# Optimization experiments

Measured on AMD Instinct MI355X. Metric: run time of the kernel, lower is better.

## Reference

```python
import jax, jax.numpy as jnp
import numpy as np

HUMAN_CONF = 0.7
KP_CONF = 0.5
NMS_THR = 0.5


def _cxcywh_to_xyxy(b):
    cx, cy, w, h = b[..., 0], b[..., 1], b[..., 2], b[..., 3]
    return jnp.stack([cx - 0.5 * w, cy - 0.5 * h, cx + 0.5 * w, cy + 0.5 * h], axis=-1)


def _iou_matrix(boxes):  # [Q,4] xyxy -> [Q,Q]
    area = jnp.maximum(boxes[:, 2] - boxes[:, 0], 0) * jnp.maximum(boxes[:, 3] - boxes[:, 1], 0)
    lt = jnp.maximum(boxes[:, None, :2], boxes[None, :, :2])
    rb = jnp.minimum(boxes[:, None, 2:], boxes[None, :, 2:])
    wh = jnp.maximum(rb - lt, 0)
    inter = wh[..., 0] * wh[..., 1]
    union = area[:, None] + area[None, :] - inter
    return inter / jnp.maximum(union, 1e-9)


def _nms(boxes, scores, valid, thr):
    # Greedy NMS over score-sorted boxes; invalid boxes never kept.
    Q = scores.shape[0]
    order = jnp.argsort(jnp.where(valid, scores, -jnp.inf))[::-1]
    b, v = boxes[order], valid[order]
    iou = _iou_matrix(b)
    idxs = jnp.arange(Q)

    def body(sup, i):
        keep_i = v[i] & jnp.logical_not(sup[i])
        sup = sup | (keep_i & (iou[i] > thr) & (idxs != i))
        return sup, keep_i

    _, keeps = jax.lax.scan(body, jnp.zeros(Q, bool), idxs)
    return jnp.zeros(Q, bool).at[order].set(keeps)


def _roi_kps(hm, box, sx, sy):
    # hm: [K,H,W] float, box: [4] int32 (xyxy in image coords).
    # Masked full-map argmax == ROI-crop argmax of the original (outside = -inf).
    K, H, W = hm.shape
    x1 = jnp.maximum((box[0].astype(jnp.float32) * sx).astype(jnp.int32), 0)
    y1 = jnp.maximum((box[1].astype(jnp.float32) * sy).astype(jnp.int32), 0)
    x2 = jnp.minimum((box[2].astype(jnp.float32) * sx).astype(jnp.int32) + 1, W)
    y2 = jnp.minimum((box[3].astype(jnp.float32) * sy).astype(jnp.int32) + 1, H)
    xs, ys = jnp.arange(W), jnp.arange(H)
    mask = ((ys >= y1) & (ys < y2))[:, None] & ((xs >= x1) & (xs < x2))[None, :]
    flat = jnp.where(mask[None], hm, -jnp.inf).reshape(K, -1)
    max_vals = flat.max(-1)
    idx = flat.argmax(-1)
    col = (idx % W).astype(jnp.float32)
    row = (idx // W).astype(jnp.float32)
    kps = jnp.stack([col / sx, row / sy, max_vals], -1)  # [K,3]
    ok = (x2 > x1) & (y2 > y1)
    return jnp.where(ok, kps, 0.0)


def setup_inputs() -> dict:
    key = jax.random.key(0)
    k1, k2, k3 = jax.random.split(key, 3)
    B, Q, K, Hh, Wh = 4, 100, 17, 128, 128
    return {
        "human_logits": jax.random.normal(k1, (B, Q, 2), jnp.float32) * 2.0,
        "pred_boxes": jax.random.uniform(k2, (B, Q, 4), jnp.float32),
        "pred_heatmaps": jax.random.normal(k3, (B, K, Hh, Wh), jnp.float32),
        "img_h": 512,
        "img_w": 512,
    }


def reference(human_logits, pred_boxes, pred_heatmaps, img_h, img_w):
    K, Hh, Wh = pred_heatmaps.shape[1:]
    prob = jax.nn.softmax(human_logits, -1)
    scores = prob.max(-1)          # [B,Q]
    labels = prob.argmax(-1)       # [B,Q]
    scale = jnp.array([img_w, img_h, img_w, img_h], jnp.float32)
    boxes = _cxcywh_to_xyxy(pred_boxes) * scale  # [B,Q,4] image coords
    valid = (labels == 0) & (scores >= HUMAN_CONF)
    keep = jax.vmap(lambda b, s, v: _nms(b, s, v, NMS_THR))(boxes, scores, valid)  # [B,Q] bool
    boxes_int = boxes.astype(jnp.int32)
    sx, sy = Wh / img_w, Hh / img_h
    kps = jax.vmap(lambda hm, bx: jax.vmap(lambda b: _roi_kps(hm, b, sx, sy))(bx))(
        pred_heatmaps, boxes_int)  # [B,Q,K,3]
    conf = kps[..., 2]
    kps = kps.at[..., 2].set(jnp.where(conf < KP_CONF, 0.0, conf))
    keep_f = keep.astype(jnp.float32)
    scores_out = scores * keep_f
    kps_out = kps * keep_f[:, :, None, None]
    boxes_out = boxes_int * keep[:, :, None]
    return scores_out, boxes_out, kps_out, keep
```

## Files before the change

### kernel.cpp

```cpp
#include <hip/hip_runtime.h>
#include <cmath>
#include <cfloat>

constexpr int NB = 4;
constexpr int NQ = 100;
constexpr int NK = 17;
constexpr int NH = 128;
constexpr int NW = 128;

constexpr float HUMAN_CONF = 0.7f;
constexpr float KP_CONF    = 0.5f;
constexpr float NMS_THR    = 0.5f;

constexpr int OFF_BOXES = NB * NQ;
constexpr int OFF_KPS   = NB * NQ * 5;
constexpr int OFF_KEEP  = NB * NQ * 5 + NB * NQ * NK * 3;

__global__ __launch_bounds__(128) void score_nms_kernel(
    const float* __restrict__ logits,
    const float* __restrict__ pboxes,
    const int* __restrict__ img_h_p,
    const int* __restrict__ img_w_p,
    float* __restrict__ out,
    int* __restrict__ wcount,
    int2* __restrict__ wlist)
{
    const int b = blockIdx.x;
    const int t = threadIdx.x;

    __shared__ float sbx[NQ][4];
    __shared__ float ssc[NQ];
    __shared__ unsigned char sval[NQ];
    __shared__ int   sorder[NQ];
    __shared__ float sortb[NQ][4];
    __shared__ float sarea[NQ];
    __shared__ unsigned char ssv[NQ];
    __shared__ unsigned long long smask0[NQ], smask1[NQ];
    __shared__ unsigned long long skmask[2];
    __shared__ unsigned long long svb[2];
    __shared__ unsigned long long swl0;

    {
        float4* kz4 = (float4*)(out + OFF_KPS + b * (NQ * NK * 3));
        const float4 z4 = make_float4(0.0f, 0.0f, 0.0f, 0.0f);
        for (int i = t; i < (NQ * NK * 3) / 4; i += 128) kz4[i] = z4;
    }

    const float iw = (float)img_w_p[0];
    const float ih = (float)img_h_p[0];
    const float sx = (float)NW / iw;
    const float sy = (float)NH / ih;

    if (t < NQ) {
        const float l0 = logits[(b * NQ + t) * 2 + 0];
        const float l1 = logits[(b * NQ + t) * 2 + 1];
        const float m  = fmaxf(l0, l1);
        const float e0 = expf(l0 - m);
        const float e1 = expf(l1 - m);
        const float score = fmaxf(e0, e1) / (e0 + e1);
        const bool  lab0  = (l0 >= l1);

        const float cx = pboxes[(b * NQ + t) * 4 + 0];
        const float cy = pboxes[(b * NQ + t) * 4 + 1];
        const float w  = pboxes[(b * NQ + t) * 4 + 2];
        const float h  = pboxes[(b * NQ + t) * 4 + 3];
        sbx[t][0] = (cx - 0.5f * w) * iw;
        sbx[t][1] = (cy - 0.5f * h) * ih;
        sbx[t][2] = (cx + 0.5f * w) * iw;
        sbx[t][3] = (cy + 0.5f * h) * ih;
        ssc[t]  = score;
        sval[t] = (lab0 && score >= HUMAN_CONF) ? 1 : 0;
    }
    __syncthreads();

    if (t < NQ) {
        const float key = sval[t] ? ssc[t] : -INFINITY;
        int rank = 0;
        for (int j = 0; j < NQ; ++j) {
            const float kj = sval[j] ? ssc[j] : -INFINITY;
            if (kj > key || (kj == key && j > t)) rank++;
        }
        sorder[rank] = t;
    }
    __syncthreads();

    if (t < NQ) {
        const int oi = sorder[t];
        const float x1 = sbx[oi][0], y1 = sbx[oi][1], x2 = sbx[oi][2], y2 = sbx[oi][3];
        sortb[t][0] = x1; sortb[t][1] = y1; sortb[t][2] = x2; sortb[t][3] = y2;
        sarea[t] = fmaxf(x2 - x1, 0.0f) * fmaxf(y2 - y1, 0.0f);
        ssv[t]   = sval[oi];
    }
    __syncthreads();

    if (t < NQ) {
        unsigned long long m0 = 0ull, m1 = 0ull;
        const float ax1 = sortb[t][0], ay1 = sortb[t][1], ax2 = sortb[t][2], ay2 = sortb[t][3];
        const float aa = sarea[t];
        for (int j = 0; j < NQ; ++j) {
            const float lx = fmaxf(ax1, sortb[j][0]);
            const float ly = fmaxf(ay1, sortb[j][1]);
            const float rx = fminf(ax2, sortb[j][2]);
            const float ry = fminf(ay2, sortb[j][3]);
            const float wv = fmaxf(rx - lx, 0.0f);
            const float hv = fmaxf(ry - ly, 0.0f);
            const float inter = wv * hv;
            const float uni = aa + sarea[j] - inter;
            const float iou = inter / fmaxf(uni, 1e-9f);
            if (iou > NMS_THR) {
                if (j < 64) m0 |= 1ull << j; else m1 |= 1ull << (j - 64);
            }
        }
        smask0[t] = m0; smask1[t] = m1;
    }

    {
        const bool sv = (t < NQ) ? (ssv[t] != 0) : false;
        const unsigned long long vb = __ballot(sv);
        if ((t & 63) == 0) svb[t >> 6] = vb;
    }
    __syncthreads();

    if (t == 0) {
        unsigned long long rem0 = svb[0], rem1 = svb[1];
        unsigned long long k0 = 0ull, k1 = 0ull;
        while (rem0 | rem1) {
            int i;
            unsigned long long bit0 = 0ull, bit1 = 0ull;
            if (rem0) { i = __builtin_ctzll(rem0); bit0 = 1ull << i; }
            else      { const int j = __builtin_ctzll(rem1); i = 64 + j; bit1 = 1ull << j; }
            k0 |= bit0; k1 |= bit1;
            rem0 &= ~(smask0[i] | bit0);
            rem1 &= ~(smask1[i] | bit1);
        }
        skmask[0] = k0; skmask[1] = k1;
    }
    __syncthreads();

    int  kp = 0, gi = 0;
    int  x1i = 0, y1i = 0, x2i = 0, y2i = 0;
    bool live = false;

    if (t < NQ) {
        const int oi = sorder[t];
        kp = (t < 64) ? (int)((skmask[0] >> t) & 1ull)
                      : (int)((skmask[1] >> (t - 64)) & 1ull);
        gi = b * NQ + oi;

        out[gi] = ssc[oi] * (float)kp;

        const int bi0 = (int)sbx[oi][0];
        const int bi1 = (int)sbx[oi][1];
        const int bi2 = (int)sbx[oi][2];
        const int bi3 = (int)sbx[oi][3];
        out[OFF_BOXES + gi * 4 + 0] = (float)(bi0 * kp);
        out[OFF_BOXES + gi * 4 + 1] = (float)(bi1 * kp);
        out[OFF_BOXES + gi * 4 + 2] = (float)(bi2 * kp);
        out[OFF_BOXES + gi * 4 + 3] = (float)(bi3 * kp);

        out[OFF_KEEP + gi] = (float)kp;

        x1i = max((int)((float)bi0 * sx), 0);
        y1i = max((int)((float)bi1 * sy), 0);
        x2i = min((int)((float)bi2 * sx) + 1, NW);
        y2i = min((int)((float)bi3 * sy) + 1, NH);
        live = kp && (x2i > x1i) && (y2i > y1i);
    }

    const unsigned long long lm = __ballot(live);
    if (t == 0) swl0 = lm;
    __syncthreads();
    if (t == 64) wcount[b] = __popcll(swl0) + __popcll(lm);
    const int lane = t & 63;
    const unsigned long long below = lm & ((lane ? (1ull << lane) : 1ull) - 1ull);
    const int rank = (t < 64) ? __popcll(below) : __popcll(swl0) + __popcll(below);
    if (live) {
        const int pack = x1i | (y1i << 8) | (x2i << 16) | (y2i << 24);
        wlist[b * NQ + rank] = make_int2(pack, gi);
    }
}

__global__ __launch_bounds__(64) void kps_kernel(
    const float* __restrict__ hm,
    const int* __restrict__ wcount,
    const int2* __restrict__ wlist,
    const int* __restrict__ img_h_p,
    const int* __restrict__ img_w_p,
    float* __restrict__ out)
{
    const int c0 = wcount[0] * NK;
    const int c1 = wcount[1] * NK;
    const int c2 = wcount[2] * NK;
    const int c3 = wcount[3] * NK;
    const int t0 = c0, t1 = c0 + c1, t2 = t1 + c2, T = t2 + c3;

    const int lane = threadIdx.x;
    const float sx = (float)NW / (float)img_w_p[0];
    const float sy = (float)NH / (float)img_h_p[0];

    for (int item = blockIdx.x; item < T; item += gridDim.x) {
        int b, base;
        if (item < t1) { if (item < t0) { b = 0; base = 0;  } else { b = 1; base = t0; } }
        else           { if (item < t2) { b = 2; base = t1; } else { b = 3; base = t2; } }
        const int local = item - base;
        const int r = local / NK;
        const int k = local - r * NK;

        const int2 wl = wlist[b * NQ + r];
        const int x1 = wl.x & 255;
        const int y1 = (wl.x >> 8) & 255;
        const int x2 = (wl.x >> 16) & 255;
        const int y2 = (wl.x >> 24) & 255;
        const int gi = wl.y;

        const float4* __restrict__ b4 =
            (const float4*)(hm + (size_t)(b * NK + k) * (NH * NW));

        const int xa     = x1 & ~3;
        const int C4     = (x2 - xa + 3) >> 2;
        const int R      = y2 - y1;
        const int total4 = R * C4;
        const unsigned M = (C4 > 1) ? (0xFFFFFFFFu / (unsigned)C4 + 1u) : 0u;

        float best = -INFINITY;
        int   bidx = 0x7fffffff;

        auto proc = [&](int idx, float4 v) {
            const int row = (C4 == 1) ? idx : (int)__umulhi((unsigned)idx, M);
            const int xb  = xa + (idx - row * C4) * 4;
            const int g   = (y1 + row) * NW + xb;
            const float v0 = (xb + 0 >= x1 && xb + 0 < x2) ? v.x : -INFINITY;
            const float v1 = (xb + 1 >= x1 && xb + 1 < x2) ? v.y : -INFINITY;
            const float v2 = (xb + 2 >= x1 && xb + 2 < x2) ? v.z : -INFINITY;
            const float v3 = (xb + 3 < x2) ? v.w : -INFINITY;
            if (v0 > best) { best = v0; bidx = g + 0; }
            if (v1 > best) { best = v1; bidx = g + 1; }
            if (v2 > best) { best = v2; bidx = g + 2; }
            if (v3 > best) { best = v3; bidx = g + 3; }
        };
        auto caddr = [&](int idx) {
            const int row = (C4 == 1) ? idx : (int)__umulhi((unsigned)idx, M);
            return (y1 + row) * (NW / 4) + (xa >> 2) + (idx - row * C4);
        };

        int idx = lane;
        for (; idx + 192 < total4; idx += 256) {
            const int a0 = caddr(idx), a1 = caddr(idx + 64), a2 = caddr(idx + 128), a3 = caddr(idx + 192);
            const float4 v0 = b4[a0];
            const float4 v1 = b4[a1];
            const float4 v2 = b4[a2];
            const float4 v3 = b4[a3];
            proc(idx, v0);
            proc(idx + 64, v1);
            proc(idx + 128, v2);
            proc(idx + 192, v3);
        }
        for (; idx < total4; idx += 64) proc(idx, b4[caddr(idx)]);

        for (int off = 32; off >= 1; off >>= 1) {
            const float ov = __shfl_down(best, off);
            const int   oi = __shfl_down(bidx, off);
            if (ov > best || (ov == best && oi < bidx)) { best = ov; bidx = oi; }
        }

        if (lane == 0) {
            const int col = bidx & (NW - 1);
            const int row = bidx >> 7;
            float conf = best;
            if (conf < KP_CONF) conf = 0.0f;
            float* kout = out + OFF_KPS + (size_t)gi * (NK * 3) + k * 3;
            kout[0] = (float)col / sx;
            kout[1] = (float)row / sy;
            kout[2] = conf;
        }
    }
}

extern "C" void kernel_launch(void* const* d_in, const int* in_sizes, int n_in,
                              void* d_out, int out_size, void* d_ws, size_t ws_size,
                              hipStream_t stream) {
    const float* logits = (const float*)d_in[0];
    const float* pboxes = (const float*)d_in[1];
    const float* hm     = (const float*)d_in[2];
    const int*   img_h  = (const int*)d_in[3];
    const int*   img_w  = (const int*)d_in[4];
    float* out = (float*)d_out;

    int*  wcount = (int*)d_ws;
    int2* wlist  = (int2*)((char*)d_ws + 256);

    score_nms_kernel<<<NB, 128, 0, stream>>>(logits, pboxes, img_h, img_w, out, wcount, wlist);
    kps_kernel<<<2048, 64, 0, stream>>>(hm, wcount, wlist, img_h, img_w, out);
}
```

Measured before the change: 106.6 us.

## Fuse scoring/NMS and keypoint ROI argmax into one kernel with redundant per-block NMS

Merges the two kernels into one launch of 1024 blocks. Each block redundantly recomputes softmax, sorting and NMS for its batch, then processes a strided slice of (query, keypoint) items straight from a shared-memory ROI pack table, which removes the workspace handoff and the second launch. Each thread also issues one float4 heatmap load per 64-byte line early to warm the cache while NMS runs. Suppressed queries write zeros directly instead of using a separate zero-fill pass. The cost is NMS duplicated 256 times per batch and a fixed work split that ignores how many boxes are actually live.

```diff
diff --git a/kernel.cpp b/kernel.cpp
--- a/kernel.cpp
+++ b/kernel.cpp
@@ -16,17 +16,21 @@
 constexpr int OFF_KPS   = NB * NQ * 5;
 constexpr int OFF_KEEP  = NB * NQ * 5 + NB * NQ * NK * 3;
 
-__global__ __launch_bounds__(128) void score_nms_kernel(
+constexpr int NBLK = 1024;
+constexpr int WAVES_PER_BATCH = (NBLK / NB) * 2;
+
+__global__ __launch_bounds__(128) void fused_kernel(
     const float* __restrict__ logits,
     const float* __restrict__ pboxes,
+    const float* __restrict__ hm,
     const int* __restrict__ img_h_p,
     const int* __restrict__ img_w_p,
-    float* __restrict__ out,
-    int* __restrict__ wcount,
-    int2* __restrict__ wlist)
+    float* __restrict__ out)
 {
-    const int b = blockIdx.x;
-    const int t = threadIdx.x;
+    const int blk = blockIdx.x;
+    const int t   = threadIdx.x;
+    const int b   = blk & 3;
+    const int sub = blk >> 2;
 
     __shared__ float sbx[NQ][4];
     __shared__ float ssc[NQ];
@@ -38,18 +42,17 @@
     __shared__ unsigned long long smask0[NQ], smask1[NQ];
     __shared__ unsigned long long skmask[2];
     __shared__ unsigned long long svb[2];
-    __shared__ unsigned long long swl0;
-
-    {
-        float4* kz4 = (float4*)(out + OFF_KPS + b * (NQ * NK * 3));
-        const float4 z4 = make_float4(0.0f, 0.0f, 0.0f, 0.0f);
-        for (int i = t; i < (NQ * NK * 3) / 4; i += 128) kz4[i] = z4;
-    }
+    __shared__ int sqpack[NQ];
+
+    float4 wv4 = make_float4(0.f, 0.f, 0.f, 0.f);
+    const int  line = blk * 128 + t;
+    const bool doW  = line < (NB * NK * NH * NW) / 16;
+    if (doW) wv4 = ((const float4*)hm)[line * 4];
 
     const float iw = (float)img_w_p[0];
     const float ih = (float)img_h_p[0];
-    const float sx = (float)NW / iw;
-    const float sy = (float)NH / ih;
+    const float sxl = (float)NW / iw;
+    const float syl = (float)NH / ih;
 
     if (t < NQ) {
         const float l0 = logits[(b * NQ + t) * 2 + 0];
@@ -137,81 +140,57 @@
     }
     __syncthreads();
 
-    int  kp = 0, gi = 0;
-    int  x1i = 0, y1i = 0, x2i = 0, y2i = 0;
-    bool live = false;
-
     if (t < NQ) {
         const int oi = sorder[t];
-        kp = (t < 64) ? (int)((skmask[0] >> t) & 1ull)
-                      : (int)((skmask[1] >> (t - 64)) & 1ull);
-        gi = b * NQ + oi;
-
-        out[gi] = ssc[oi] * (float)kp;
+        const int kp = (t < 64) ? (int)((skmask[0] >> t) & 1ull)
+                                : (int)((skmask[1] >> (t - 64)) & 1ull);
 
         const int bi0 = (int)sbx[oi][0];
         const int bi1 = (int)sbx[oi][1];
         const int bi2 = (int)sbx[oi][2];
         const int bi3 = (int)sbx[oi][3];
-        out[OFF_BOXES + gi * 4 + 0] = (float)(bi0 * kp);
-        out[OFF_BOXES + gi * 4 + 1] = (float)(bi1 * kp);
-        out[OFF_BOXES + gi * 4 + 2] = (float)(bi2 * kp);
-        out[OFF_BOXES + gi * 4 + 3] = (float)(bi3 * kp);
-
-        out[OFF_KEEP + gi] = (float)kp;
-
-        x1i = max((int)((float)bi0 * sx), 0);
-        y1i = max((int)((float)bi1 * sy), 0);
-        x2i = min((int)((float)bi2 * sx) + 1, NW);
-        y2i = min((int)((float)bi3 * sy) + 1, NH);
-        live = kp && (x2i > x1i) && (y2i > y1i);
-    }
-
-    const unsigned long long lm = __ballot(live);
-    if (t == 0) swl0 = lm;
-    __syncthreads();
-    if (t == 64) wcount[b] = __popcll(swl0) + __popcll(lm);
+
+        const int x1i = max((int)((float)bi0 * sxl), 0);
+        const int y1i = max((int)((float)bi1 * syl), 0);
+        const int x2i = min((int)((float)bi2 * sxl) + 1, NW);
+        const int y2i = min((int)((float)bi3 * syl) + 1, NH);
+        const bool live = kp && (x2i > x1i) && (y2i > y1i);
+
+        sqpack[oi] = live ? (x1i | (y1i << 8) | (x2i << 16) | (y2i << 24)) : 0;
+
+        if (sub == 0) {
+            const int gi = b * NQ + oi;
+            out[gi] = ssc[oi] * (float)kp;
+            out[OFF_BOXES + gi * 4 + 0] = (float)(bi0 * kp);
+            out[OFF_BOXES + gi * 4 + 1] = (float)(bi1 * kp);
+            out[OFF_BOXES + gi * 4 + 2] = (float)(bi2 * kp);
+            out[OFF_BOXES + gi * 4 + 3] = (float)(bi3 * kp);
+            out[OFF_KEEP + gi] = (float)kp;
+        }
+    }
+    __syncthreads();
+
+    if (doW) asm volatile("" :: "v"(wv4.x), "v"(wv4.y), "v"(wv4.z), "v"(wv4.w));
+
     const int lane = t & 63;
-    const unsigned long long below = lm & ((lane ? (1ull << lane) : 1ull) - 1ull);
-    const int rank = (t < 64) ? __popcll(below) : __popcll(swl0) + __popcll(below);
-    if (live) {
-        const int pack = x1i | (y1i << 8) | (x2i << 16) | (y2i << 24);
-        wlist[b * NQ + rank] = make_int2(pack, gi);
-    }
-}
-
-__global__ __launch_bounds__(64) void kps_kernel(
-    const float* __restrict__ hm,
-    const int* __restrict__ wcount,
-    const int2* __restrict__ wlist,
-    const int* __restrict__ img_h_p,
-    const int* __restrict__ img_w_p,
-    float* __restrict__ out)
-{
-    const int c0 = wcount[0] * NK;
-    const int c1 = wcount[1] * NK;
-    const int c2 = wcount[2] * NK;
-    const int c3 = wcount[3] * NK;
-    const int t0 = c0, t1 = c0 + c1, t2 = t1 + c2, T = t2 + c3;
-
-    const int lane = threadIdx.x;
-    const float sx = (float)NW / (float)img_w_p[0];
-    const float sy = (float)NH / (float)img_h_p[0];
-
-    for (int item = blockIdx.x; item < T; item += gridDim.x) {
-        int b, base;
-        if (item < t1) { if (item < t0) { b = 0; base = 0;  } else { b = 1; base = t0; } }
-        else           { if (item < t2) { b = 2; base = t1; } else { b = 3; base = t2; } }
-        const int local = item - base;
-        const int r = local / NK;
-        const int k = local - r * NK;
-
-        const int2 wl = wlist[b * NQ + r];
-        const int x1 = wl.x & 255;
-        const int y1 = (wl.x >> 8) & 255;
-        const int x2 = (wl.x >> 16) & 255;
-        const int y2 = (wl.x >> 24) & 255;
-        const int gi = wl.y;
+    const int wvid = sub * 2 + (t >> 6);
+
+    for (int item = wvid; item < NQ * NK; item += WAVES_PER_BATCH) {
+        const int q = item / NK;
+        const int k = item - q * NK;
+        const int gi = b * NQ + q;
+        float* kout = out + OFF_KPS + (size_t)gi * (NK * 3) + k * 3;
+
+        const int pack = sqpack[q];
+        if (pack == 0) {
+            if (lane < 3) kout[lane] = 0.0f;
+            continue;
+        }
+
+        const int x1 = pack & 255;
+        const int y1 = (pack >> 8) & 255;
+        const int x2 = (pack >> 16) & 255;
+        const int y2 = (pack >> 24) & 255;
 
         const float4* __restrict__ b4 =
             (const float4*)(hm + (size_t)(b * NK + k) * (NH * NW));
@@ -268,9 +247,8 @@
             const int row = bidx >> 7;
             float conf = best;
             if (conf < KP_CONF) conf = 0.0f;
-            float* kout = out + OFF_KPS + (size_t)gi * (NK * 3) + k * 3;
-            kout[0] = (float)col / sx;
-            kout[1] = (float)row / sy;
+            kout[0] = (float)col / sxl;
+            kout[1] = (float)row / syl;
             kout[2] = conf;
         }
     }
@@ -286,9 +264,5 @@
     const int*   img_w  = (const int*)d_in[4];
     float* out = (float*)d_out;
 
-    int*  wcount = (int*)d_ws;
-    int2* wlist  = (int2*)((char*)d_ws + 256);
-
-    score_nms_kernel<<<NB, 128, 0, stream>>>(logits, pboxes, img_h, img_w, out, wcount, wlist);
-    kps_kernel<<<2048, 64, 0, stream>>>(hm, wcount, wlist, img_h, img_w, out);
+    fused_kernel<<<NBLK, 128, 0, stream>>>(logits, pboxes, hm, img_h, img_w, out);
 }
```

Result: no change. 105.8 us (-0.7%).
